# Optimization experiments

Hardware: AMD Instinct MI355X
Metric: run time of the kernel (lower is better)

## Reference

```python
import jax, jax.numpy as jnp
import numpy as np

B, V, D = 4096, 20, 768


def _conv1d_k3(x, w, b):
    # x: [B, V, D]; single-channel conv1d, kernel=3, padding=1 (torch cross-correlation)
    xp = jnp.pad(x, ((0, 0), (0, 0), (1, 1)))
    return w[0] * xp[..., :-2] + w[1] * xp[..., 1:-1] + w[2] * xp[..., 2:] + b[0]


def setup_inputs() -> dict:
    key = jax.random.key(0)
    ks = jax.random.split(key, 10)
    s = 0.02  # small init scale for weights
    return {
        "text_features": jax.random.normal(ks[0], (B, D), jnp.float32),
        "viewport_features": jax.random.normal(ks[1], (B, V, D), jnp.float32),
        "W1": jax.random.normal(ks[2], (D, D), jnp.float32) * s,
        "b1": jax.random.normal(ks[3], (D,), jnp.float32) * s,
        "W2": jax.random.normal(ks[4], (D, D), jnp.float32) * s,
        "b2": jax.random.normal(ks[5], (D,), jnp.float32) * s,
        "cw1": jax.random.normal(ks[6], (3,), jnp.float32) * 0.5,
        "cb1": jax.random.normal(ks[7], (1,), jnp.float32) * 0.1,
        "cw2": jax.random.normal(ks[8], (3,), jnp.float32) * 0.5,
        "cb2": jax.random.normal(ks[9], (1,), jnp.float32) * 0.1,
    }


def reference(text_features, viewport_features, W1, b1, W2, b2, cw1, cb1, cw2, cb2):
    # Batched over all 20 viewports at once (original loops over i).
    fli_norm = jax.nn.softmax(viewport_features, axis=-1)          # [B,V,D]
    # torch Linear: x @ W.T + b
    m1 = jnp.einsum('bvd,ed->bve', fli_norm, W1) + b1              # mlp1(fli_norm)
    m2 = jnp.einsum('bvd,ed->bve', fli_norm, W2) + b2              # mlp2(fli_norm)
    fused = jax.nn.relu(text_features[:, None, :] * m1 + m2)       # [B,V,D]
    fused = _conv1d_k3(fused, cw1, cb1)
    fused = jax.nn.relu(fused)
    fused = _conv1d_k3(fused, cw2, cb2)
    return fused.reshape(B, V * D)                                 # torch.cat along dim=1
```

## Files before the change

kernel.cpp:

```cpp
#include <hip/hip_runtime.h>

typedef unsigned short u16;
typedef unsigned char u8;
typedef __attribute__((ext_vector_type(8))) short short8;
typedef __attribute__((ext_vector_type(4))) float f32x4;

#define Bn 4096
#define Vn 20
#define Dn 768
#define Mn (Bn * Vn)
#define Nn (2 * Dn)

#define BM 256
#define BNt 256
#define NTILES (Nn / BNt)
#define GRID ((Mn / BM) * NTILES)

#define SCL 32.0f
#define ISCL2 (1.0f / 1024.0f)

typedef __attribute__((address_space(1))) void GV;
typedef __attribute__((address_space(3))) void LV;

__device__ __forceinline__ u16 f2bf(float f) {
  union { float f; unsigned u; } v; v.f = f;
  unsigned r = v.u + 0x7FFFu + ((v.u >> 16) & 1u);
  return (u16)(r >> 16);
}
__device__ __forceinline__ float bf2f(u16 x) {
  union { unsigned u; float f; } v; v.u = ((unsigned)x) << 16; return v.f;
}

__device__ __forceinline__ int lds8(int r, int hi) {
  return (r >> 2) * 128 + (r & 3) * 32 + ((((hi >> 1) ^ ((r >> 2) & 1))) << 4)
         + (hi & 1) * 8;
}

__global__ __launch_bounds__(192) void softmax_k(const float* __restrict__ vf,
                                                 u8* __restrict__ X8) {
  size_t row = blockIdx.x;
  const float4* p = (const float4*)(vf + row * Dn);
  int t = threadIdx.x;
  float4 v = p[t];
  float mx = fmaxf(fmaxf(v.x, v.y), fmaxf(v.z, v.w));
  #pragma unroll
  for (int off = 32; off; off >>= 1) mx = fmaxf(mx, __shfl_xor(mx, off));
  __shared__ float rr[3];
  __shared__ float rs[3];
  int wv = t >> 6, ln = t & 63;
  if (!ln) rr[wv] = mx;
  __syncthreads();
  mx = fmaxf(fmaxf(rr[0], rr[1]), rr[2]);
  float e0 = __expf(v.x - mx), e1 = __expf(v.y - mx);
  float e2 = __expf(v.z - mx), e3 = __expf(v.w - mx);
  float s = e0 + e1 + e2 + e3;
  #pragma unroll
  for (int off = 32; off; off >>= 1) s += __shfl_xor(s, off);
  if (!ln) rs[wv] = s;
  __syncthreads();
  float inv = SCL / (rs[0] + rs[1] + rs[2]);
  unsigned pk = 0;
  pk = __builtin_amdgcn_cvt_pk_fp8_f32(e0 * inv, e1 * inv, pk, false);
  pk = __builtin_amdgcn_cvt_pk_fp8_f32(e2 * inv, e3 * inv, pk, true);
  ((unsigned*)(X8 + row * Dn))[t] = pk;
}

__global__ __launch_bounds__(256) void build_wt_k(const float* __restrict__ W1,
                                                  const float* __restrict__ W2,
                                                  u8* __restrict__ Wt8) {
  int idx = blockIdx.x * 256 + threadIdx.x;
  if (idx >= Dn * (Dn / 4)) return;
  int j = idx / (Dn / 4), d4 = (idx - j * (Dn / 4)) * 4;
  int b = j >> 5, c = j & 31;
  float4 a = *(const float4*)(W1 + (size_t)j * Dn + d4);
  float4 e = *(const float4*)(W2 + (size_t)j * Dn + d4);
  unsigned p1 = 0, p2 = 0;
  p1 = __builtin_amdgcn_cvt_pk_fp8_f32(a.x * SCL, a.y * SCL, p1, false);
  p1 = __builtin_amdgcn_cvt_pk_fp8_f32(a.z * SCL, a.w * SCL, p1, true);
  p2 = __builtin_amdgcn_cvt_pk_fp8_f32(e.x * SCL, e.y * SCL, p2, false);
  p2 = __builtin_amdgcn_cvt_pk_fp8_f32(e.z * SCL, e.w * SCL, p2, true);
  *(unsigned*)(Wt8 + (size_t)(b * 64 + c) * Dn + d4)      = p1;
  *(unsigned*)(Wt8 + (size_t)(b * 64 + 32 + c) * Dn + d4) = p2;
}

__global__ __launch_bounds__(512, 2) void gemm_fuse_k(
    const u8* __restrict__ X8, const u8* __restrict__ Wt8,
    const float* __restrict__ b1, const float* __restrict__ b2,
    const float* __restrict__ text, float* __restrict__ out,
    u16* __restrict__ seam,
    const float* __restrict__ cw1, const float* __restrict__ cb1,
    const float* __restrict__ cw2, const float* __restrict__ cb2) {
  __shared__ __align__(16) u16 smem[65536];
  u8* smem8 = (u8*)smem;

  const int h = blockIdx.x;
  const int lin = (h & 7) * (GRID / 8) + (h >> 3);
  const int by = lin / NTILES, bx = lin - by * NTILES;
  const int brow = by * BM;

  const int t = threadIdx.x, w = t >> 6, l = t & 63;
  const int lo = l & 15, hi = l >> 4;
  const int wrr = w >> 2, wcc = w & 3;

  int offA[8], offB[4];
  #pragma unroll
  for (int m = 0; m < 8; ++m) offA[m] = lds8(wrr * 128 + m * 16 + lo, hi);
  #pragma unroll
  for (int n = 0; n < 4; ++n) offB[n] = lds8(wcc * 64 + n * 16 + lo, hi);

  const u8* gA;
  const u8* gB;
  {
    int r = (t >> 3) * 4 + ((t & 7) >> 1);
    int c16 = (t & 1) ^ ((t >> 3) & 1);
    gA = X8 + (size_t)(brow + r) * Dn + c16 * 16;
    gB = Wt8 + (size_t)(bx * BNt + r) * Dn + c16 * 16;
  }

#define STG_A(DST, KOFF) __builtin_amdgcn_global_load_lds( \
    (GV*)(gA + (KOFF)), (LV*)(smem8 + (DST) + w * 1024), 16, 0, 0)
#define STG_B(DST, KOFF) __builtin_amdgcn_global_load_lds( \
    (GV*)(gB + (KOFF)), (LV*)(smem8 + (DST) + w * 1024), 16, 0, 0)

  STG_A(0, 0);              STG_B(16384, 0);
  STG_A(32768, 64);         STG_B(49152, 64);
  STG_A(8192, 32);          STG_B(24576, 32);
  STG_A(40960, 96);         STG_B(57344, 96);
  asm volatile("s_waitcnt vmcnt(6)" ::: "memory");
  __builtin_amdgcn_s_barrier();

  f32x4 acc[8][4] = {};
  long af[8], bb0, bb1;

#define PH(SB, KH, NH, NEWA, STG, VM) do {                                     \
    if (NEWA) { _Pragma("unroll") for (int m = 0; m < 8; ++m)                  \
      af[m] = *(const long*)(smem8 + (SB) + (KH) * 8192 + offA[m]); }          \
    bb0 = *(const long*)(smem8 + (SB) + 16384 + (KH) * 8192 + offB[(NH)*2]);   \
    bb1 = *(const long*)(smem8 + (SB) + 16384 + (KH) * 8192 + offB[(NH)*2+1]); \
    STG;                                                                       \
    __builtin_amdgcn_s_barrier();                                              \
    asm volatile("s_waitcnt lgkmcnt(0)" ::: "memory");                         \
    __builtin_amdgcn_sched_barrier(0);                                         \
    __builtin_amdgcn_s_setprio(1);                                             \
    _Pragma("unroll") for (int m = 0; m < 8; ++m) {                            \
      acc[m][(NH)*2]   = __builtin_amdgcn_mfma_f32_16x16x32_fp8_fp8(af[m], bb0, acc[m][(NH)*2],   0, 0, 0); \
      acc[m][(NH)*2+1] = __builtin_amdgcn_mfma_f32_16x16x32_fp8_fp8(af[m], bb1, acc[m][(NH)*2+1], 0, 0, 0); \
    }                                                                          \
    __builtin_amdgcn_s_setprio(0);                                             \
    VM;                                                                        \
    __builtin_amdgcn_s_barrier();                                              \
  } while (0)

#define VM2 asm volatile("s_waitcnt vmcnt(2)" ::: "memory")
#define VM0 asm volatile("s_waitcnt vmcnt(0)" ::: "memory")

  #pragma unroll
  for (int i = 0; i < 6; ++i) {
    const int ka = (2 * i + 1) * 64;
    const int kb = (2 * i + 2) * 64;
    PH(0, 0, 0, true,  if (i >= 1) STG_A(32768, ka),      ;  );
    PH(0, 0, 1, false, if (i >= 1) STG_B(49152, ka),      VM2);
    PH(0, 1, 0, true,  if (i >= 1) STG_A(40960, ka + 32), ;  );
    PH(0, 1, 1, false, if (i >= 1) STG_B(57344, ka + 32), VM2);
    PH(32768, 0, 0, true,  if (i <= 4) STG_A(0, kb),          ;  );
    PH(32768, 0, 1, false, if (i <= 4) STG_B(16384, kb),      if (i == 5) { VM0; } else { VM2; });
    PH(32768, 1, 0, true,  if (i <= 4) STG_A(8192, kb + 32),  ;  );
    PH(32768, 1, 1, false, if (i <= 4) STG_B(24576, kb + 32), if (i <= 4) { VM2; });
  }
#undef PH
#undef VM2
#undef VM0
#undef STG_A
#undef STG_B

  const float w10 = cw1[0], w11 = cw1[1], w12 = cw1[2], c1b = cb1[0];
  const float w20 = cw2[0], w21 = cw2[1], w22 = cw2[2], c2b = cb2[0];

  u16* fsm = smem;
  u16* tsm = smem + 32768;

  #pragma unroll
  for (int n = 0; n < 2; ++n) {
    const int cl = wcc * 32 + n * 16 + lo;
    const int e  = bx * 128 + cl;
    const float B1 = b1[e], B2 = b2[e];
    #pragma unroll
    for (int m = 0; m < 8; ++m) {
      const int rl = wrr * 128 + m * 16 + hi * 4;
      uint2 pk;
      u16* pku = (u16*)&pk;
      #pragma unroll
      for (int r = 0; r < 4; ++r) {
        const int gr = brow + rl + r;
        const float v1 = acc[m][n][r] * ISCL2 + B1;
        const float v2 = acc[m][n + 2][r] * ISCL2 + B2;
        const float tf = text[(size_t)(gr / Vn) * Dn + e];
        pku[r] = f2bf(fmaxf(tf * v1 + v2, 0.0f));
      }
      *(uint2*)(fsm + cl * 256 + (rl ^ ((cl & 31) << 3))) = pk;
      const int sidx = (cl < 4) ? cl : ((cl >= 124) ? cl - 120 : -1);
      if (sidx >= 0)
        *(uint2*)(seam + ((size_t)(by * 6 + bx) * 8 + sidx) * 256 + rl) = pk;
    }
  }
  __syncthreads();

  const int cl = t & 127, rb = t >> 7;
  const int cL = cl ? cl - 1 : 0, cR = (cl < 127) ? cl + 1 : 127;
  short8 tC[8];
  #pragma unroll
  for (int j = 0; j < 8; ++j) {
    const int R = rb * 64 + j * 8;
    short8 sL = *(const short8*)(fsm + cL * 256 + (R ^ ((cL & 31) << 3)));
    short8 sC = *(const short8*)(fsm + cl * 256 + (R ^ ((cl & 31) << 3)));
    short8 sR = *(const short8*)(fsm + cR * 256 + (R ^ ((cR & 31) << 3)));
    short8 o;
    #pragma unroll
    for (int k = 0; k < 8; ++k) {
      float a = bf2f((u16)sL[k]), b = bf2f((u16)sC[k]), c = bf2f((u16)sR[k]);
      float v = fmaxf(fmaf(w10, a, fmaf(w11, b, fmaf(w12, c, c1b))), 0.0f);
      o[k] = (short)f2bf(v);
    }
    *(short8*)(tsm + cl * 256 + (R ^ ((cl & 31) << 3))) = o;
    tC[j] = o;
  }
  __syncthreads();

  const bool wr_ok = (cl >= 2 && cl <= 125);
  #pragma unroll
  for (int j = 0; j < 8; ++j) {
    const int R = rb * 64 + j * 8;
    short8 tL = *(const short8*)(tsm + cL * 256 + (R ^ ((cL & 31) << 3)));
    short8 tR = *(const short8*)(tsm + cR * 256 + (R ^ ((cR & 31) << 3)));
    #pragma unroll
    for (int k = 0; k < 8; ++k) {
      float v = fmaf(w20, bf2f((u16)tL[k]),
                fmaf(w21, bf2f((u16)tC[j][k]),
                fmaf(w22, bf2f((u16)tR[k]), c2b)));
      if (wr_ok)
        out[(size_t)(brow + R + k) * Dn + bx * 128 + cl] = v;
    }
  }
}

__global__ __launch_bounds__(256) void seam_k(const u16* __restrict__ seam,
                                              float* __restrict__ out,
                                              const float* __restrict__ cw1,
                                              const float* __restrict__ cb1,
                                              const float* __restrict__ cw2,
                                              const float* __restrict__ cb2) {
  const int bid = blockIdx.x;
  const int by = bid / 6, bx = bid - by * 6;
  const int r = threadIdx.x;
  const float w10 = cw1[0], w11 = cw1[1], w12 = cw1[2], c1b = cb1[0];
  const float w20 = cw2[0], w21 = cw2[1], w22 = cw2[2], c2b = cb2[0];
  #define SM(B, I) bf2f(seam[((size_t)(B) * 8 + (I)) * 256 + r])
  float fm2 = 0.f, fm1 = 0.f, fR0 = 0.f, fR1 = 0.f;
  if (bx > 0) { fm2 = SM(bid - 1, 6); fm1 = SM(bid - 1, 7); }
  if (bx < 5) { fR0 = SM(bid + 1, 0); fR1 = SM(bid + 1, 1); }
  const float f0 = SM(bid, 0), f1 = SM(bid, 1), f2 = SM(bid, 2), f3 = SM(bid, 3);
  const float f124 = SM(bid, 4), f125 = SM(bid, 5), f126 = SM(bid, 6), f127 = SM(bid, 7);
  #undef SM
  #define C1(a, b, c) fmaxf(fmaf(w10, (a), fmaf(w11, (b), fmaf(w12, (c), c1b))), 0.0f)
  const float tm1  = (bx > 0) ? C1(fm2, fm1, f0) : 0.0f;
  const float t0   = C1(fm1, f0, f1);
  const float t1   = C1(f0, f1, f2);
  const float t2   = C1(f1, f2, f3);
  const float t125 = C1(f124, f125, f126);
  const float t126 = C1(f125, f126, f127);
  const float t127 = C1(f126, f127, fR0);
  const float t128 = (bx < 5) ? C1(f127, fR0, fR1) : 0.0f;
  #undef C1
  const size_t go = (size_t)(by * 256 + r) * Dn + bx * 128;
  out[go + 0]   = fmaf(w20, tm1,  fmaf(w21, t0,   fmaf(w22, t1,   c2b)));
  out[go + 1]   = fmaf(w20, t0,   fmaf(w21, t1,   fmaf(w22, t2,   c2b)));
  out[go + 126] = fmaf(w20, t125, fmaf(w21, t126, fmaf(w22, t127, c2b)));
  out[go + 127] = fmaf(w20, t126, fmaf(w21, t127, fmaf(w22, t128, c2b)));
}

extern "C" void kernel_launch(void* const* d_in, const int* in_sizes, int n_in,
                              void* d_out, int out_size, void* d_ws, size_t ws_size,
                              hipStream_t stream) {
  const float* text = (const float*)d_in[0];
  const float* vf   = (const float*)d_in[1];
  const float* W1   = (const float*)d_in[2];
  const float* b1   = (const float*)d_in[3];
  const float* W2   = (const float*)d_in[4];
  const float* b2   = (const float*)d_in[5];
  const float* cw1  = (const float*)d_in[6];
  const float* cb1  = (const float*)d_in[7];
  const float* cw2  = (const float*)d_in[8];
  const float* cb2  = (const float*)d_in[9];
  float* out = (float*)d_out;

  u8*  X8   = (u8*)d_ws;
  u8*  Wt8  = X8 + (size_t)Mn * Dn;
  u16* seam = (u16*)(Wt8 + (size_t)Nn * Dn);

  softmax_k<<<Mn, 192, 0, stream>>>(vf, X8);
  build_wt_k<<<(Dn * (Dn / 4) + 255) / 256, 256, 0, stream>>>(W1, W2, Wt8);
  gemm_fuse_k<<<GRID, 512, 0, stream>>>(X8, Wt8, b1, b2, text, out, seam,
                                        cw1, cb1, cw2, cb2);
  seam_k<<<GRID, 256, 0, stream>>>(seam, out, cw1, cb1, cw2, cb2);
}
```

Measured before the change: 346.6 us.

## Pre-tile fp8 activations and weights into LDS-ready panel layout for contiguous loads

The softmax and weight-build kernels now write fp8 data in a panel-tiled order (256-row panels, 32-byte k-slices, 8-byte planes) that matches the GEMM's LDS fragment layout. Each global_load_lds in the GEMM becomes a fully contiguous 8 KB slice per k-step instead of strided row reads, and the XOR-swizzled LDS addressing is replaced by a plain linear offset. The aim is better global-load coalescing and simpler address arithmetic. The trade-offs are scattered 4-byte writes in the producer kernels and possible LDS bank conflicts now that the swizzle is gone.

Result: slower. 375.7 us (+8.4%).

```diff
diff --git a/kernel.cpp b/kernel.cpp
--- a/kernel.cpp
+++ b/kernel.cpp
@@ -15,6 +15,7 @@
 #define BNt 256
 #define NTILES (Nn / BNt)
 #define GRID ((Mn / BM) * NTILES)
+#define PANEL (256 * Dn)
 
 #define SCL 32.0f
 #define ISCL2 (1.0f / 1024.0f)
@@ -31,10 +32,6 @@
   union { unsigned u; float f; } v; v.u = ((unsigned)x) << 16; return v.f;
 }
 
-__device__ __forceinline__ int lds8(int r, int hi) {
-  return (r >> 2) * 128 + (r & 3) * 32 + ((((hi >> 1) ^ ((r >> 2) & 1))) << 4)
-         + (hi & 1) * 8;
-}
 
 __global__ __launch_bounds__(192) void softmax_k(const float* __restrict__ vf,
                                                  u8* __restrict__ X8) {
@@ -62,7 +59,10 @@
   unsigned pk = 0;
   pk = __builtin_amdgcn_cvt_pk_fp8_f32(e0 * inv, e1 * inv, pk, false);
   pk = __builtin_amdgcn_cvt_pk_fp8_f32(e2 * inv, e3 * inv, pk, true);
-  ((unsigned*)(X8 + row * Dn))[t] = pk;
+  const int q = (int)(row & 255);
+  u8* dst = X8 + (row >> 8) * PANEL + (size_t)(t >> 3) * 8192
+            + ((t >> 1) & 3) * 2048 + (q >> 1) * 16 + (q & 1) * 8 + (t & 1) * 4;
+  *(unsigned*)dst = pk;
 }
 
 __global__ __launch_bounds__(256) void build_wt_k(const float* __restrict__ W1,
@@ -79,8 +79,13 @@
   p1 = __builtin_amdgcn_cvt_pk_fp8_f32(a.z * SCL, a.w * SCL, p1, true);
   p2 = __builtin_amdgcn_cvt_pk_fp8_f32(e.x * SCL, e.y * SCL, p2, false);
   p2 = __builtin_amdgcn_cvt_pk_fp8_f32(e.z * SCL, e.w * SCL, p2, true);
-  *(unsigned*)(Wt8 + (size_t)(b * 64 + c) * Dn + d4)      = p1;
-  *(unsigned*)(Wt8 + (size_t)(b * 64 + 32 + c) * Dn + d4) = p2;
+  const int slice = d4 >> 5, plane = (d4 >> 3) & 3, bb = d4 & 7;
+  const int j1 = b * 64 + c, j2 = b * 64 + 32 + c;
+  const int q1 = j1 & 255, q2 = j2 & 255;
+  *(unsigned*)(Wt8 + (size_t)(j1 >> 8) * PANEL + (size_t)slice * 8192
+               + plane * 2048 + (q1 >> 1) * 16 + (q1 & 1) * 8 + bb) = p1;
+  *(unsigned*)(Wt8 + (size_t)(j2 >> 8) * PANEL + (size_t)slice * 8192
+               + plane * 2048 + (q2 >> 1) * 16 + (q2 & 1) * 8 + bb) = p2;
 }
 
 __global__ __launch_bounds__(512, 2) void gemm_fuse_k(
@@ -104,28 +109,24 @@
 
   int offA[8], offB[4];
   #pragma unroll
-  for (int m = 0; m < 8; ++m) offA[m] = lds8(wrr * 128 + m * 16 + lo, hi);
-  #pragma unroll
-  for (int n = 0; n < 4; ++n) offB[n] = lds8(wcc * 64 + n * 16 + lo, hi);
-
-  const u8* gA;
-  const u8* gB;
-  {
-    int r = (t >> 3) * 4 + ((t & 7) >> 1);
-    int c16 = (t & 1) ^ ((t >> 3) & 1);
-    gA = X8 + (size_t)(brow + r) * Dn + c16 * 16;
-    gB = Wt8 + (size_t)(bx * BNt + r) * Dn + c16 * 16;
-  }
-
-#define STG_A(DST, KOFF) __builtin_amdgcn_global_load_lds( \
-    (GV*)(gA + (KOFF)), (LV*)(smem8 + (DST) + w * 1024), 16, 0, 0)
-#define STG_B(DST, KOFF) __builtin_amdgcn_global_load_lds( \
-    (GV*)(gB + (KOFF)), (LV*)(smem8 + (DST) + w * 1024), 16, 0, 0)
+  for (int m = 0; m < 8; ++m)
+    offA[m] = hi * 2048 + (wrr * 64 + m * 8 + (lo >> 1)) * 16 + (lo & 1) * 8;
+  #pragma unroll
+  for (int n = 0; n < 4; ++n)
+    offB[n] = hi * 2048 + (wcc * 32 + n * 8 + (lo >> 1)) * 16 + (lo & 1) * 8;
+
+  const u8* gAp = X8 + (size_t)by * PANEL + t * 16;
+  const u8* gBp = Wt8 + (size_t)bx * PANEL + t * 16;
+
+#define STG_A(DST, SL) __builtin_amdgcn_global_load_lds( \
+    (GV*)(gAp + (size_t)(SL) * 8192), (LV*)(smem8 + (DST) + w * 1024), 16, 0, 0)
+#define STG_B(DST, SL) __builtin_amdgcn_global_load_lds( \
+    (GV*)(gBp + (size_t)(SL) * 8192), (LV*)(smem8 + (DST) + w * 1024), 16, 0, 0)
 
   STG_A(0, 0);              STG_B(16384, 0);
-  STG_A(32768, 64);         STG_B(49152, 64);
-  STG_A(8192, 32);          STG_B(24576, 32);
-  STG_A(40960, 96);         STG_B(57344, 96);
+  STG_A(32768, 2);          STG_B(49152, 2);
+  STG_A(8192, 1);           STG_B(24576, 1);
+  STG_A(40960, 3);          STG_B(57344, 3);
   asm volatile("s_waitcnt vmcnt(6)" ::: "memory");
   __builtin_amdgcn_s_barrier();
 
@@ -156,16 +157,16 @@
 
   #pragma unroll
   for (int i = 0; i < 6; ++i) {
-    const int ka = (2 * i + 1) * 64;
-    const int kb = (2 * i + 2) * 64;
-    PH(0, 0, 0, true,  if (i >= 1) STG_A(32768, ka),      ;  );
-    PH(0, 0, 1, false, if (i >= 1) STG_B(49152, ka),      VM2);
-    PH(0, 1, 0, true,  if (i >= 1) STG_A(40960, ka + 32), ;  );
-    PH(0, 1, 1, false, if (i >= 1) STG_B(57344, ka + 32), VM2);
-    PH(32768, 0, 0, true,  if (i <= 4) STG_A(0, kb),          ;  );
-    PH(32768, 0, 1, false, if (i <= 4) STG_B(16384, kb),      if (i == 5) { VM0; } else { VM2; });
-    PH(32768, 1, 0, true,  if (i <= 4) STG_A(8192, kb + 32),  ;  );
-    PH(32768, 1, 1, false, if (i <= 4) STG_B(24576, kb + 32), if (i <= 4) { VM2; });
+    const int sa = 2 * (2 * i + 1);
+    const int sb = 2 * (2 * i + 2);
+    PH(0, 0, 0, true,  if (i >= 1) STG_A(32768, sa),     ;  );
+    PH(0, 0, 1, false, if (i >= 1) STG_B(49152, sa),     VM2);
+    PH(0, 1, 0, true,  if (i >= 1) STG_A(40960, sa + 1), ;  );
+    PH(0, 1, 1, false, if (i >= 1) STG_B(57344, sa + 1), VM2);
+    PH(32768, 0, 0, true,  if (i <= 4) STG_A(0, sb),         ;  );
+    PH(32768, 0, 1, false, if (i <= 4) STG_B(16384, sb),     if (i == 5) { VM0; } else { VM2; });
+    PH(32768, 1, 0, true,  if (i <= 4) STG_A(8192, sb + 1),  ;  );
+    PH(32768, 1, 1, false, if (i <= 4) STG_B(24576, sb + 1), if (i <= 4) { VM2; });
   }
 #undef PH
 #undef VM2
```
